# Optimization experiments

Hardware: AMD Instinct MI355X
Metric: run time of the kernel (lower is better)

## Reference

```python
import jax, jax.numpy as jnp
import numpy as np

B, N, C, F = 8, 3, 64, 128
H = W = 128


def _up2(x):
    # nearest-neighbor upsample by 2 on the last two axes
    return jnp.repeat(jnp.repeat(x, 2, axis=-2), 2, axis=-1)


def setup_inputs() -> dict:
    key = jax.random.key(0)
    ks = jax.random.split(key, 12)
    s = lambda k, shp, fan: jax.random.normal(k, shp, jnp.float32) * (1.0 / np.sqrt(fan))
    return {
        "contexts": jax.random.normal(ks[0], (B, N, C, H, W), jnp.float32),
        "mainstream": jax.random.normal(ks[1], (B, F, H // 2, W // 2), jnp.float32),
        "Wc": s(ks[2], (C, C), C),        # W_context 1x1 conv weight [out,in]
        "bc": jnp.zeros((C,), jnp.float32),
        "Wf": s(ks[3], (C, F), F),        # W_feat 1x1
        "bf": jnp.zeros((C,), jnp.float32),
        "Wk": s(ks[4], (C, F), F),        # W_key_feat 1x1
        "bk": jnp.zeros((C,), jnp.float32),
        "Vw": s(ks[5], (C, F, 3, 3), F * 9),  # values_conv 3x3, OIHW
        "Vb": jnp.zeros((C,), jnp.float32),
    }


def reference(contexts, mainstream, Wc, bc, Wf, bf, Wk, bk, Vw, Vb):
    # contexts: [B,N,C,H,W], mainstream: [B,F,h,w]
    bias = lambda b: b[None, :, None, None]
    queries = jnp.einsum('bfhw,cf->bchw', mainstream, Wf) + bias(bf)       # [B,C,h,w]
    keys_m = jnp.einsum('bfhw,cf->bchw', mainstream, Wk) + bias(bk)        # [B,C,h,w]
    values = jax.lax.conv_general_dilated(
        mainstream, Vw, (1, 1), 'SAME',
        dimension_numbers=('NCHW', 'OIHW', 'NCHW')) + bias(Vb)             # [B,C,h,w]

    # stack contexts with upsampled mainstream keys, project with W_context (1x1)
    keys_stack = jnp.concatenate([contexts, _up2(keys_m)[:, None]], axis=1)  # [B,N+1,C,H,W]
    keys_proj = jnp.einsum('bnchw,dc->bndhw', keys_stack, Wc) + bc[None, None, :, None, None]

    q_up = _up2(queries)                                                    # [B,C,H,W]
    logits = jnp.einsum('bnchw,bchw->bnhw', keys_proj, q_up)                # [B,N+1,H,W]
    attn = jax.nn.softmax(logits, axis=1)                                   # softmax over contexts

    vals_stack = jnp.concatenate([contexts, _up2(values)[:, None]], axis=1) # [B,N+1,C,H,W]
    out = jnp.einsum('bnchw,bnhw->bchw', vals_stack, attn)                  # [B,C,H,W]
    return out
```

## Files before the change

### kernel.cpp

```cpp
#include <hip/hip_runtime.h>
#include <math.h>

#define CH   64
#define FD   128
#define HS   64
#define FS   128
#define NB   8
#define NCTX 3

#define WS_QT   0
#define WS_VAL  2097152
#define WS_L3   4194304
#define WS_BQ   4227072
#define WS_AVH  4227136
#define WS_AQH  4264000
#define WS_AQL  4268096
#define WS_AKH  4272192
#define WS_AKL  4276288

typedef short  s16x8  __attribute__((ext_vector_type(8)));
typedef float  f32x16 __attribute__((ext_vector_type(16)));

__device__ inline unsigned short bf16_rne(float x) {
  unsigned u = __float_as_uint(x);
  u += 0x7FFFu + ((u >> 16) & 1u);
  return (unsigned short)(u >> 16);
}
__device__ inline void split2(float x, unsigned short& h, unsigned short& l) {
  h = bf16_rne(x);
  l = bf16_rne(x - __uint_as_float((unsigned)h << 16));
}

__global__ __launch_bounds__(256) void afrag_prep(
    const float* __restrict__ Wc, const float* __restrict__ Wf,
    const float* __restrict__ bf, const float* __restrict__ Wk,
    const float* __restrict__ Vw, float* __restrict__ ws) {
  int id = blockIdx.x * 256 + threadIdx.x;
  unsigned short* avh = (unsigned short*)(ws + WS_AVH);
  unsigned short* aqh = (unsigned short*)(ws + WS_AQH);
  unsigned short* aql = (unsigned short*)(ws + WS_AQL);
  unsigned short* akh = (unsigned short*)(ws + WS_AKH);
  unsigned short* akl = (unsigned short*)(ws + WS_AKL);

  if (id < 9216) {
    int tile = id / 4608, rem = id % 4608;
    int q = rem >> 6, l = rem & 63;
    int am = l & 31, kh = l >> 5;
    int c = tile * 32 + am, tap = q >> 3, kf = q & 7;
#pragma unroll
    for (int j = 0; j < 8; ++j) {
      int f = kf * 16 + kh * 8 + j;
      avh[id * 8 + j] = bf16_rne(Vw[(c * FD + f) * 9 + tap]);
    }
  } else if (id < 10240) {
    int i2 = id - 9216;
    int tile = i2 >> 9, rem = i2 & 511;
    int q = rem >> 6, l = rem & 63;
    int am = l & 31, kh = l >> 5;
    int c = tile * 32 + am;
#pragma unroll
    for (int j = 0; j < 8; ++j) {
      int f = q * 16 + kh * 8 + j;
      float acc = 0.f;
      for (int d = 0; d < CH; ++d)
        acc = fmaf(Wc[d * CH + c], Wf[d * FD + f], acc);
      unsigned short h, lo; split2(acc, h, lo);
      aqh[i2 * 8 + j] = h; aql[i2 * 8 + j] = lo;
    }
  } else if (id < 11264) {
    int i3 = id - 10240;
    int tile = i3 >> 9, rem = i3 & 511;
    int q = rem >> 6, l = rem & 63;
    int am = l & 31, kh = l >> 5;
    int c = tile * 32 + am;
#pragma unroll
    for (int j = 0; j < 8; ++j) {
      int f = q * 16 + kh * 8 + j;
      unsigned short h, lo; split2(Wk[c * FD + f], h, lo);
      akh[i3 * 8 + j] = h; akl[i3 * 8 + j] = lo;
    }
  } else if (id < 11328) {
    int c = id - 11264;
    float acc = 0.f;
    for (int d = 0; d < CH; ++d) acc = fmaf(Wc[d * CH + c], bf[d], acc);
    ws[WS_BQ + c] = acc;
  }
}

__global__ __launch_bounds__(512) void half_fused(
    const float* __restrict__ m, const float* __restrict__ Vb,
    const float* __restrict__ bk, float* __restrict__ ws) {
  const int b = blockIdx.x >> 6, y = blockIdx.x & 63;
  const int t = threadIdx.x, lane = t & 63;
  const int wave = __builtin_amdgcn_readfirstlane(t >> 6);
  const int am = lane & 31, kh = lane >> 5;

  __shared__ __align__(16) short HI[3][8][66][2][8];
  __shared__ float l3red[2][64];

  if (t < 96) {
    int row = t / 32, kf = (t >> 2) & 7, khh = (t >> 1) & 1, col = (t & 1) * 65;
    s16x8 z;
#pragma unroll
    for (int j = 0; j < 8; ++j) z[j] = 0;
    *(s16x8*)&HI[row][kf][col][khh][0] = z;
  }

#pragma unroll
  for (int i = 0; i < 6; ++i) {
    const int tk = wave * 6 + i;
    const int row = tk >> 4, kf = (tk >> 1) & 7, khh = tk & 1;
    const int yy = y + row - 1;
    s16x8 hi;
    if (yy >= 0 && yy < HS) {
#pragma unroll
      for (int j = 0; j < 8; ++j) {
        const int f = kf * 16 + khh * 8 + j;
        hi[j] = (short)bf16_rne(m[((b * FD + f) * HS + yy) * HS + lane]);
      }
    } else {
#pragma unroll
      for (int j = 0; j < 8; ++j) hi[j] = 0;
    }
    *(s16x8*)&HI[row][kf][lane + 1][khh][0] = hi;
  }
  __syncthreads();

  float l3part = 0.f;
  if (wave < 4) {
    const int ct = wave >> 1, xh = wave & 1;
    const int x0 = xh * 32, ch0 = ct * 32;
    const unsigned short* avh = (const unsigned short*)(ws + WS_AVH);
    f32x16 acc;
#pragma unroll
    for (int i = 0; i < 16; ++i) acc[i] = 0.f;
#pragma unroll 8
    for (int q = 0; q < 72; ++q) {
      const int tap = q >> 3, kf = q & 7;
      const s16x8 ah = *(const s16x8*)(avh + ((ct * 72 + q) * 64 + lane) * 8);
      const s16x8 bh = *(const s16x8*)&HI[tap / 3][kf][x0 + am + tap % 3][kh][0];
      acc = __builtin_amdgcn_mfma_f32_32x32x16_bf16(ah, bh, acc, 0, 0, 0);
    }
#pragma unroll
    for (int r = 0; r < 16; ++r) {
      const int c = ch0 + (r & 3) + 8 * (r >> 2) + 4 * kh;
      ws[WS_VAL + ((b * CH + c) * HS + y) * HS + x0 + am] = acc[r] + Vb[c];
    }
  } else {
    const int w4 = wave - 4;
    const int ct = w4 >> 1, xh = w4 & 1;
    const int x0 = xh * 32, ch0 = ct * 32;
    const unsigned short* aqh = (const unsigned short*)(ws + WS_AQH);
    const unsigned short* aql = (const unsigned short*)(ws + WS_AQL);
    const unsigned short* akh = (const unsigned short*)(ws + WS_AKH);
    const unsigned short* akl = (const unsigned short*)(ws + WS_AKL);
    f32x16 q1, q2, k1, k2;
#pragma unroll
    for (int i = 0; i < 16; ++i) { q1[i] = 0.f; q2[i] = 0.f; k1[i] = 0.f; k2[i] = 0.f; }
#pragma unroll
    for (int q = 0; q < 8; ++q) {
      const s16x8 bh = *(const s16x8*)&HI[1][q][x0 + am + 1][kh][0];
      s16x8 bl;
#pragma unroll
      for (int j = 0; j < 8; ++j) {
        const float mv = m[((b * FD + q * 16 + kh * 8 + j) * HS + y) * HS + x0 + am];
        const float hf = __uint_as_float(((unsigned)(unsigned short)bh[j]) << 16);
        bl[j] = (short)bf16_rne(mv - hf);
      }
      const s16x8 ah = *(const s16x8*)(aqh + ((ct * 8 + q) * 64 + lane) * 8);
      const s16x8 al = *(const s16x8*)(aql + ((ct * 8 + q) * 64 + lane) * 8);
      const s16x8 kah = *(const s16x8*)(akh + ((ct * 8 + q) * 64 + lane) * 8);
      const s16x8 kal = *(const s16x8*)(akl + ((ct * 8 + q) * 64 + lane) * 8);
      q1 = __builtin_amdgcn_mfma_f32_32x32x16_bf16(ah, bh, q1, 0, 0, 0);
      q1 = __builtin_amdgcn_mfma_f32_32x32x16_bf16(al, bh, q1, 0, 0, 0);
      q2 = __builtin_amdgcn_mfma_f32_32x32x16_bf16(ah, bl, q2, 0, 0, 0);
      k1 = __builtin_amdgcn_mfma_f32_32x32x16_bf16(kah, bh, k1, 0, 0, 0);
      k1 = __builtin_amdgcn_mfma_f32_32x32x16_bf16(kal, bh, k1, 0, 0, 0);
      k2 = __builtin_amdgcn_mfma_f32_32x32x16_bf16(kah, bl, k2, 0, 0, 0);
    }
#pragma unroll
    for (int r = 0; r < 16; ++r) {
      const int c = ch0 + (r & 3) + 8 * (r >> 2) + 4 * kh;
      const float qv = q1[r] + q2[r] + ws[WS_BQ + c];
      const float kv = k1[r] + k2[r] + bk[c];
      ws[WS_QT + ((b * CH + c) * HS + y) * HS + x0 + am] = qv;
      l3part = fmaf(qv, kv, l3part);
    }
    if (ct == 1) l3red[xh][lane] = l3part;
  }
  __syncthreads();

  if (wave == 4 || wave == 5) {
    const int xh = wave - 4;
    float s = l3part + l3red[xh][lane];
    s += __shfl_xor(s, 32, 64);
    if (kh == 0)
      ws[WS_L3 + (b * HS + y) * HS + xh * 32 + am] = s;
  }
}

__global__ __launch_bounds__(256) void fullres_kernel(
    const float* __restrict__ ctx, const float* __restrict__ ws,
    float* __restrict__ out) {
  const int xh = blockIdx.x & 1, hrow = blockIdx.x >> 1;
  const int b = blockIdx.y;
  const int quad = threadIdx.x & 15;
  const int cg = threadIdx.x >> 4;
  const int x = xh * 64 + quad * 4;
  const int h2 = hrow >> 1, w2 = (x >> 1);
  const int c0 = cg * 4;

  const size_t cbase = (size_t)(b * NCTX * CH) * FS * FS + hrow * FS + x;
  const int cs = FS * FS, ns = CH * FS * FS;

  float4 cv[3][4];
  float2 qv[4];
#pragma unroll
  for (int j = 0; j < 4; ++j) {
    const int c = c0 + j;
    cv[0][j] = *(const float4*)(ctx + cbase + c * cs);
    cv[1][j] = *(const float4*)(ctx + cbase + ns + c * cs);
    cv[2][j] = *(const float4*)(ctx + cbase + 2 * ns + c * cs);
    qv[j] = *(const float2*)(ws + WS_QT + (size_t)(b * CH + c) * HS * HS + h2 * HS + w2);
  }

  float4 pl[3];
#pragma unroll
  for (int n = 0; n < 3; ++n) {
    pl[n].x = pl[n].y = pl[n].z = pl[n].w = 0.f;
#pragma unroll
    for (int j = 0; j < 4; ++j) {
      pl[n].x = fmaf(cv[n][j].x, qv[j].x, pl[n].x);
      pl[n].y = fmaf(cv[n][j].y, qv[j].x, pl[n].y);
      pl[n].z = fmaf(cv[n][j].z, qv[j].y, pl[n].z);
      pl[n].w = fmaf(cv[n][j].w, qv[j].y, pl[n].w);
    }
  }

  __shared__ float4 part[3][16][17];
  __shared__ float  Lred[3][64];
#pragma unroll
  for (int n = 0; n < 3; ++n) part[n][cg][quad] = pl[n];
  __syncthreads();

  {
    const int tt = threadIdx.x;
    if (tt < 192) {
      const int n = tt >> 6, px = tt & 63;
      const float* pp = (const float*)part + (size_t)n * 16 * 17 * 4 + px;
      float s = 0.f;
#pragma unroll
      for (int g = 0; g < 16; ++g) s += pp[g * 68];
      Lred[n][px] = s;
    }
  }
  __syncthreads();

  float4 Lv0 = *(const float4*)&Lred[0][quad * 4];
  float4 Lv1 = *(const float4*)&Lred[1][quad * 4];
  float4 Lv2 = *(const float4*)&Lred[2][quad * 4];
  float2 l3v = *(const float2*)(ws + WS_L3 + (b * HS + h2) * HS + w2);

  float A0[4], A1[4], A2[4], A3[4];
  const float* L0p = (const float*)&Lv0;
  const float* L1p = (const float*)&Lv1;
  const float* L2p = (const float*)&Lv2;
#pragma unroll
  for (int k = 0; k < 4; ++k) {
    float L0 = L0p[k], L1 = L1p[k], L2 = L2p[k];
    float L3 = (k < 2) ? l3v.x : l3v.y;
    float mx = fmaxf(fmaxf(L0, L1), fmaxf(L2, L3));
    float e0 = __expf(L0 - mx), e1 = __expf(L1 - mx);
    float e2 = __expf(L2 - mx), e3 = __expf(L3 - mx);
    float inv = 1.f / (e0 + e1 + e2 + e3);
    A0[k] = e0 * inv; A1[k] = e1 * inv; A2[k] = e2 * inv; A3[k] = e3 * inv;
  }

  float* op = out + (size_t)(b * CH) * FS * FS + hrow * FS + x;
#pragma unroll
  for (int j = 0; j < 4; ++j) {
    const int c = c0 + j;
    float2 vv = *(const float2*)(ws + WS_VAL + (size_t)(b * CH + c) * HS * HS + h2 * HS + w2);
    float4 o;
    o.x = fmaf(A0[0], cv[0][j].x, fmaf(A1[0], cv[1][j].x, fmaf(A2[0], cv[2][j].x, A3[0] * vv.x)));
    o.y = fmaf(A0[1], cv[0][j].y, fmaf(A1[1], cv[1][j].y, fmaf(A2[1], cv[2][j].y, A3[1] * vv.x)));
    o.z = fmaf(A0[2], cv[0][j].z, fmaf(A1[2], cv[1][j].z, fmaf(A2[2], cv[2][j].z, A3[2] * vv.y)));
    o.w = fmaf(A0[3], cv[0][j].w, fmaf(A1[3], cv[1][j].w, fmaf(A2[3], cv[2][j].w, A3[3] * vv.y)));
    *(float4*)(op + c * cs) = o;
  }
}

extern "C" void kernel_launch(void* const* d_in, const int* in_sizes, int n_in,
                              void* d_out, int out_size, void* d_ws, size_t ws_size,
                              hipStream_t stream) {
  const float* ctx = (const float*)d_in[0];
  const float* ms  = (const float*)d_in[1];
  const float* Wc  = (const float*)d_in[2];
  const float* Wf  = (const float*)d_in[4];
  const float* bf  = (const float*)d_in[5];
  const float* Wk  = (const float*)d_in[6];
  const float* bk  = (const float*)d_in[7];
  const float* Vw  = (const float*)d_in[8];
  const float* Vb  = (const float*)d_in[9];
  float* ws  = (float*)d_ws;
  float* out = (float*)d_out;

  afrag_prep<<<45, 256, 0, stream>>>(Wc, Wf, bf, Wk, Vw, ws);
  half_fused<<<NB * HS, 512, 0, stream>>>(ms, Vb, bk, ws);
  fullres_kernel<<<dim3(2 * FS, NB), 256, 0, stream>>>(ctx, ws, out);
}
```

Measured before the change: 249.7 us.

## Fuse half-resolution projections with full-resolution attention into one kernel

Merges the half-res conv/projection kernel and the full-res softmax-attention kernel into one kernel per (batch, half-res row). Queries, values and the mainstream-key logit stay in shared memory (union with the bf16 staging buffer) instead of making a round trip through global workspace. The cross-channel logit reduction now uses wave shuffles plus a small shared buffer. In exchange each block handles two full-res rows serially, with more syncs and larger shared memory, which may lower occupancy and the overlap of context streaming.

```diff
diff --git a/kernel.cpp b/kernel.cpp
--- a/kernel.cpp
+++ b/kernel.cpp
@@ -8,9 +8,6 @@
 #define NB   8
 #define NCTX 3
 
-#define WS_QT   0
-#define WS_VAL  2097152
-#define WS_L3   4194304
 #define WS_BQ   4227072
 #define WS_AVH  4227136
 #define WS_AQH  4264000
@@ -87,15 +84,24 @@
   }
 }
 
-__global__ __launch_bounds__(512) void half_fused(
+__global__ __launch_bounds__(512) void fused_kernel(
     const float* __restrict__ m, const float* __restrict__ Vb,
-    const float* __restrict__ bk, float* __restrict__ ws) {
+    const float* __restrict__ bk, const float* __restrict__ ctx,
+    float* __restrict__ out, const float* __restrict__ ws) {
   const int b = blockIdx.x >> 6, y = blockIdx.x & 63;
   const int t = threadIdx.x, lane = t & 63;
   const int wave = __builtin_amdgcn_readfirstlane(t >> 6);
   const int am = lane & 31, kh = lane >> 5;
 
-  __shared__ __align__(16) short HI[3][8][66][2][8];
+  __shared__ __align__(16) union {
+    short HI[3][8][66][2][8];
+    struct {
+      float  QT[CH * HS];
+      float  VAL[CH * HS];
+      float4 wpart[2][4][3][16];
+      float  L3row[HS];
+    } p;
+  } U;
   __shared__ float l3red[2][64];
 
   if (t < 96) {
@@ -103,7 +109,7 @@
     s16x8 z;
 #pragma unroll
     for (int j = 0; j < 8; ++j) z[j] = 0;
-    *(s16x8*)&HI[row][kf][col][khh][0] = z;
+    *(s16x8*)&U.HI[row][kf][col][khh][0] = z;
   }
 
 #pragma unroll
@@ -122,44 +128,38 @@
 #pragma unroll
       for (int j = 0; j < 8; ++j) hi[j] = 0;
     }
-    *(s16x8*)&HI[row][kf][lane + 1][khh][0] = hi;
+    *(s16x8*)&U.HI[row][kf][lane + 1][khh][0] = hi;
   }
   __syncthreads();
 
+  const int ct = (wave >> 1) & 1;
+  const int xh = wave & 1;
+  const int x0 = xh * 32, ch0 = ct * 32;
+
+  f32x16 acc, q1, q2, k1, k2;
   float l3part = 0.f;
+
   if (wave < 4) {
-    const int ct = wave >> 1, xh = wave & 1;
-    const int x0 = xh * 32, ch0 = ct * 32;
     const unsigned short* avh = (const unsigned short*)(ws + WS_AVH);
-    f32x16 acc;
 #pragma unroll
     for (int i = 0; i < 16; ++i) acc[i] = 0.f;
 #pragma unroll 8
     for (int q = 0; q < 72; ++q) {
       const int tap = q >> 3, kf = q & 7;
       const s16x8 ah = *(const s16x8*)(avh + ((ct * 72 + q) * 64 + lane) * 8);
-      const s16x8 bh = *(const s16x8*)&HI[tap / 3][kf][x0 + am + tap % 3][kh][0];
+      const s16x8 bh = *(const s16x8*)&U.HI[tap / 3][kf][x0 + am + tap % 3][kh][0];
       acc = __builtin_amdgcn_mfma_f32_32x32x16_bf16(ah, bh, acc, 0, 0, 0);
     }
-#pragma unroll
-    for (int r = 0; r < 16; ++r) {
-      const int c = ch0 + (r & 3) + 8 * (r >> 2) + 4 * kh;
-      ws[WS_VAL + ((b * CH + c) * HS + y) * HS + x0 + am] = acc[r] + Vb[c];
-    }
   } else {
-    const int w4 = wave - 4;
-    const int ct = w4 >> 1, xh = w4 & 1;
-    const int x0 = xh * 32, ch0 = ct * 32;
     const unsigned short* aqh = (const unsigned short*)(ws + WS_AQH);
     const unsigned short* aql = (const unsigned short*)(ws + WS_AQL);
     const unsigned short* akh = (const unsigned short*)(ws + WS_AKH);
     const unsigned short* akl = (const unsigned short*)(ws + WS_AKL);
-    f32x16 q1, q2, k1, k2;
 #pragma unroll
     for (int i = 0; i < 16; ++i) { q1[i] = 0.f; q2[i] = 0.f; k1[i] = 0.f; k2[i] = 0.f; }
 #pragma unroll
     for (int q = 0; q < 8; ++q) {
-      const s16x8 bh = *(const s16x8*)&HI[1][q][x0 + am + 1][kh][0];
+      const s16x8 bh = *(const s16x8*)&U.HI[1][q][x0 + am + 1][kh][0];
       s16x8 bl;
 #pragma unroll
       for (int j = 0; j < 8; ++j) {
@@ -178,115 +178,134 @@
       k1 = __builtin_amdgcn_mfma_f32_32x32x16_bf16(kal, bh, k1, 0, 0, 0);
       k2 = __builtin_amdgcn_mfma_f32_32x32x16_bf16(kah, bl, k2, 0, 0, 0);
     }
+  }
+  __syncthreads();
+
+  if (wave < 4) {
 #pragma unroll
     for (int r = 0; r < 16; ++r) {
       const int c = ch0 + (r & 3) + 8 * (r >> 2) + 4 * kh;
-      const float qv = q1[r] + q2[r] + ws[WS_BQ + c];
-      const float kv = k1[r] + k2[r] + bk[c];
-      ws[WS_QT + ((b * CH + c) * HS + y) * HS + x0 + am] = qv;
-      l3part = fmaf(qv, kv, l3part);
+      U.p.VAL[c * HS + x0 + am] = acc[r] + Vb[c];
+    }
+  } else {
+#pragma unroll
+    for (int r = 0; r < 16; ++r) {
+      const int c = ch0 + (r & 3) + 8 * (r >> 2) + 4 * kh;
+      const float qvv = q1[r] + q2[r] + ws[WS_BQ + c];
+      const float kvv = k1[r] + k2[r] + bk[c];
+      U.p.QT[c * HS + x0 + am] = qvv;
+      l3part = fmaf(qvv, kvv, l3part);
     }
     if (ct == 1) l3red[xh][lane] = l3part;
   }
   __syncthreads();
 
   if (wave == 4 || wave == 5) {
-    const int xh = wave - 4;
     float s = l3part + l3red[xh][lane];
     s += __shfl_xor(s, 32, 64);
-    if (kh == 0)
-      ws[WS_L3 + (b * HS + y) * HS + xh * 32 + am] = s;
-  }
-}
-
-__global__ __launch_bounds__(256) void fullres_kernel(
-    const float* __restrict__ ctx, const float* __restrict__ ws,
-    float* __restrict__ out) {
-  const int xh = blockIdx.x & 1, hrow = blockIdx.x >> 1;
-  const int b = blockIdx.y;
-  const int quad = threadIdx.x & 15;
-  const int cg = threadIdx.x >> 4;
-  const int x = xh * 64 + quad * 4;
-  const int h2 = hrow >> 1, w2 = (x >> 1);
-  const int c0 = cg * 4;
-
-  const size_t cbase = (size_t)(b * NCTX * CH) * FS * FS + hrow * FS + x;
+    if (kh == 0) U.p.L3row[x0 + am] = s;
+  }
+  __syncthreads();
+
+  const int u    = t >> 8;
+  const int tt   = t & 255;
+  const int quad = tt & 15;
+  const int cg   = tt >> 4;
+  const int wv   = tt >> 6;
+  const int c0   = cg * 4;
+  const int hrow = 2 * y + u;
   const int cs = FS * FS, ns = CH * FS * FS;
 
-  float4 cv[3][4];
-  float2 qv[4];
-#pragma unroll
-  for (int j = 0; j < 4; ++j) {
-    const int c = c0 + j;
-    cv[0][j] = *(const float4*)(ctx + cbase + c * cs);
-    cv[1][j] = *(const float4*)(ctx + cbase + ns + c * cs);
-    cv[2][j] = *(const float4*)(ctx + cbase + 2 * ns + c * cs);
-    qv[j] = *(const float2*)(ws + WS_QT + (size_t)(b * CH + c) * HS * HS + h2 * HS + w2);
-  }
-
-  float4 pl[3];
-#pragma unroll
-  for (int n = 0; n < 3; ++n) {
-    pl[n].x = pl[n].y = pl[n].z = pl[n].w = 0.f;
+  float* op = out + (size_t)(b * CH) * FS * FS + (size_t)hrow * FS;
+  const float* cb = ctx + (size_t)(b * NCTX * CH) * cs + (size_t)hrow * FS;
+
+#pragma unroll 1
+  for (int x2 = 0; x2 < 2; ++x2) {
+    const int x = x2 * 64 + quad * 4;
+    const int w2 = x >> 1;
+
+    float4 cv[3][4];
+    float2 qv[4];
 #pragma unroll
     for (int j = 0; j < 4; ++j) {
-      pl[n].x = fmaf(cv[n][j].x, qv[j].x, pl[n].x);
-      pl[n].y = fmaf(cv[n][j].y, qv[j].x, pl[n].y);
-      pl[n].z = fmaf(cv[n][j].z, qv[j].y, pl[n].z);
-      pl[n].w = fmaf(cv[n][j].w, qv[j].y, pl[n].w);
-    }
-  }
-
-  __shared__ float4 part[3][16][17];
-  __shared__ float  Lred[3][64];
-#pragma unroll
-  for (int n = 0; n < 3; ++n) part[n][cg][quad] = pl[n];
-  __syncthreads();
-
-  {
-    const int tt = threadIdx.x;
-    if (tt < 192) {
-      const int n = tt >> 6, px = tt & 63;
-      const float* pp = (const float*)part + (size_t)n * 16 * 17 * 4 + px;
-      float s = 0.f;
-#pragma unroll
-      for (int g = 0; g < 16; ++g) s += pp[g * 68];
-      Lred[n][px] = s;
-    }
-  }
-  __syncthreads();
-
-  float4 Lv0 = *(const float4*)&Lred[0][quad * 4];
-  float4 Lv1 = *(const float4*)&Lred[1][quad * 4];
-  float4 Lv2 = *(const float4*)&Lred[2][quad * 4];
-  float2 l3v = *(const float2*)(ws + WS_L3 + (b * HS + h2) * HS + w2);
-
-  float A0[4], A1[4], A2[4], A3[4];
-  const float* L0p = (const float*)&Lv0;
-  const float* L1p = (const float*)&Lv1;
-  const float* L2p = (const float*)&Lv2;
-#pragma unroll
-  for (int k = 0; k < 4; ++k) {
-    float L0 = L0p[k], L1 = L1p[k], L2 = L2p[k];
-    float L3 = (k < 2) ? l3v.x : l3v.y;
-    float mx = fmaxf(fmaxf(L0, L1), fmaxf(L2, L3));
-    float e0 = __expf(L0 - mx), e1 = __expf(L1 - mx);
-    float e2 = __expf(L2 - mx), e3 = __expf(L3 - mx);
-    float inv = 1.f / (e0 + e1 + e2 + e3);
-    A0[k] = e0 * inv; A1[k] = e1 * inv; A2[k] = e2 * inv; A3[k] = e3 * inv;
-  }
-
-  float* op = out + (size_t)(b * CH) * FS * FS + hrow * FS + x;
-#pragma unroll
-  for (int j = 0; j < 4; ++j) {
-    const int c = c0 + j;
-    float2 vv = *(const float2*)(ws + WS_VAL + (size_t)(b * CH + c) * HS * HS + h2 * HS + w2);
-    float4 o;
-    o.x = fmaf(A0[0], cv[0][j].x, fmaf(A1[0], cv[1][j].x, fmaf(A2[0], cv[2][j].x, A3[0] * vv.x)));
-    o.y = fmaf(A0[1], cv[0][j].y, fmaf(A1[1], cv[1][j].y, fmaf(A2[1], cv[2][j].y, A3[1] * vv.x)));
-    o.z = fmaf(A0[2], cv[0][j].z, fmaf(A1[2], cv[1][j].z, fmaf(A2[2], cv[2][j].z, A3[2] * vv.y)));
-    o.w = fmaf(A0[3], cv[0][j].w, fmaf(A1[3], cv[1][j].w, fmaf(A2[3], cv[2][j].w, A3[3] * vv.y)));
-    *(float4*)(op + c * cs) = o;
+      const int c = c0 + j;
+      cv[0][j] = *(const float4*)(cb + x + c * cs);
+      cv[1][j] = *(const float4*)(cb + x + ns + c * cs);
+      cv[2][j] = *(const float4*)(cb + x + 2 * ns + c * cs);
+      qv[j] = *(const float2*)&U.p.QT[c * HS + w2];
+    }
+
+    float4 pl[3];
+#pragma unroll
+    for (int n = 0; n < 3; ++n) {
+      pl[n].x = pl[n].y = pl[n].z = pl[n].w = 0.f;
+#pragma unroll
+      for (int j = 0; j < 4; ++j) {
+        pl[n].x = fmaf(cv[n][j].x, qv[j].x, pl[n].x);
+        pl[n].y = fmaf(cv[n][j].y, qv[j].x, pl[n].y);
+        pl[n].z = fmaf(cv[n][j].z, qv[j].y, pl[n].z);
+        pl[n].w = fmaf(cv[n][j].w, qv[j].y, pl[n].w);
+      }
+    }
+
+#pragma unroll
+    for (int n = 0; n < 3; ++n) {
+      pl[n].x += __shfl_xor(pl[n].x, 16, 64);
+      pl[n].y += __shfl_xor(pl[n].y, 16, 64);
+      pl[n].z += __shfl_xor(pl[n].z, 16, 64);
+      pl[n].w += __shfl_xor(pl[n].w, 16, 64);
+      pl[n].x += __shfl_xor(pl[n].x, 32, 64);
+      pl[n].y += __shfl_xor(pl[n].y, 32, 64);
+      pl[n].z += __shfl_xor(pl[n].z, 32, 64);
+      pl[n].w += __shfl_xor(pl[n].w, 32, 64);
+    }
+    __syncthreads();
+    if ((lane >> 4) == 0) {
+#pragma unroll
+      for (int n = 0; n < 3; ++n) U.p.wpart[u][wv][n][quad] = pl[n];
+    }
+    __syncthreads();
+
+    float4 L[3];
+#pragma unroll
+    for (int n = 0; n < 3; ++n) {
+      const float4 p0 = U.p.wpart[u][0][n][quad];
+      const float4 p1 = U.p.wpart[u][1][n][quad];
+      const float4 p2 = U.p.wpart[u][2][n][quad];
+      const float4 p3 = U.p.wpart[u][3][n][quad];
+      L[n].x = (p0.x + p1.x) + (p2.x + p3.x);
+      L[n].y = (p0.y + p1.y) + (p2.y + p3.y);
+      L[n].z = (p0.z + p1.z) + (p2.z + p3.z);
+      L[n].w = (p0.w + p1.w) + (p2.w + p3.w);
+    }
+    const float2 l3v = *(const float2*)&U.p.L3row[w2];
+
+    float A0[4], A1[4], A2[4], A3[4];
+    const float* L0p = (const float*)&L[0];
+    const float* L1p = (const float*)&L[1];
+    const float* L2p = (const float*)&L[2];
+#pragma unroll
+    for (int k = 0; k < 4; ++k) {
+      float L0 = L0p[k], L1 = L1p[k], L2 = L2p[k];
+      float L3 = (k < 2) ? l3v.x : l3v.y;
+      float mx = fmaxf(fmaxf(L0, L1), fmaxf(L2, L3));
+      float e0 = __expf(L0 - mx), e1 = __expf(L1 - mx);
+      float e2 = __expf(L2 - mx), e3 = __expf(L3 - mx);
+      float inv = 1.f / (e0 + e1 + e2 + e3);
+      A0[k] = e0 * inv; A1[k] = e1 * inv; A2[k] = e2 * inv; A3[k] = e3 * inv;
+    }
+
+#pragma unroll
+    for (int j = 0; j < 4; ++j) {
+      const int c = c0 + j;
+      const float2 vv = *(const float2*)&U.p.VAL[c * HS + w2];
+      float4 o;
+      o.x = fmaf(A0[0], cv[0][j].x, fmaf(A1[0], cv[1][j].x, fmaf(A2[0], cv[2][j].x, A3[0] * vv.x)));
+      o.y = fmaf(A0[1], cv[0][j].y, fmaf(A1[1], cv[1][j].y, fmaf(A2[1], cv[2][j].y, A3[1] * vv.x)));
+      o.z = fmaf(A0[2], cv[0][j].z, fmaf(A1[2], cv[1][j].z, fmaf(A2[2], cv[2][j].z, A3[2] * vv.y)));
+      o.w = fmaf(A0[3], cv[0][j].w, fmaf(A1[3], cv[1][j].w, fmaf(A2[3], cv[2][j].w, A3[3] * vv.y)));
+      *(float4*)(op + x + c * cs) = o;
+    }
   }
 }
 
@@ -306,6 +325,5 @@
   float* out = (float*)d_out;
 
   afrag_prep<<<45, 256, 0, stream>>>(Wc, Wf, bf, Wk, Vw, ws);
-  half_fused<<<NB * HS, 512, 0, stream>>>(ms, Vb, bk, ws);
-  fullres_kernel<<<dim3(2 * FS, NB), 256, 0, stream>>>(ctx, ws, out);
-}
+  fused_kernel<<<NB * HS, 512, 0, stream>>>(ms, Vb, bk, ctx, out, ws);
+}
```

After: 244.9 us. Within noise of the previous version (-1.9%).
